# Optimization experiments

Measured on AMD Instinct MI355X. Metric: run time of the kernel, lower is better.

The kernel has to match this reference:

```python
import jax, jax.numpy as jnp
import numpy as np
from jax import lax

B, T, C, H, N = 4, 1024, 2048, 32, 64
KVH = 8            # kv heads -> kv_dim = 512, n_rep = 4
GN_EPS = 0.00064   # group_norm eps from Step3


def _l2norm(x):
    # torch F.normalize(p=2, dim=-1) with eps=1e-12
    n = jnp.linalg.norm(x, axis=-1, keepdims=True)
    return x / jnp.maximum(n, 1e-12)


def _rwkv7_scan(r, decay, k, v, aa, bb, state):
    # all inputs (B,T,H,N); state (B,H,N,N) with layout [value, key]
    def step(S, inp):
        r_t, d_t, k_t, v_t, a_t, b_t = inp  # each (B,H,N)
        sa = jnp.einsum('bhik,bhk->bhi', S, a_t)
        S = (S * d_t[:, :, None, :]
             + sa[..., None] * b_t[:, :, None, :]
             + v_t[..., None] * k_t[:, :, None, :])
        y = jnp.einsum('bhik,bhk->bhi', S, r_t)
        return S, y
    xs = tuple(jnp.moveaxis(t, 1, 0) for t in (r, decay, k, v, aa, bb))  # (T,B,H,N)
    state, ys = lax.scan(step, state, xs)
    return jnp.moveaxis(ys, 0, 1), state  # (B,T,H,N), (B,H,N,N)


def _forward(x, v_first, state, R, R_bias, K, K_bias, V, V_bias, O, O_bias,
             w0, w1, w2, a0, a1, a2, v0, v1, v2, k_k, k_a, r_k, ln_w, ln_b):
    # ---- Step1: projections + gates (hybrid_matmul -> plain matmul in fp32 ref) ----
    r = x @ R.T + R_bias                                   # (B,T,C)
    w_raw = -jax.nn.softplus(-(w0 + jnp.tanh(x @ w1) @ w2)) - 0.6
    k = x @ K.T + K_bias                                   # (B,T,512)
    v = x @ V.T + V_bias
    n_rep = C // K.shape[0]
    k = jnp.repeat(k.reshape(B, T, KVH, N), n_rep, axis=2).reshape(B, T, C)
    v = jnp.repeat(v.reshape(B, T, KVH, N), n_rep, axis=2).reshape(B, T, C)
    a = jax.nn.sigmoid(a0 + (x @ a1) @ a2)
    kk = _l2norm((k * k_k).reshape(B, T, H, N)).reshape(B, T, C)
    k = k * (1.0 + (a - 1.0) * k_a)
    # layer_id != 0: cross-layer value blending
    v = v + (v_first - v) * jax.nn.sigmoid(v0 + (x @ v1) @ v2)
    aa = -kk
    bb = kk * a
    # ---- Step2: fused recurrent rwkv7 (fp32 state) ----
    decay = jnp.exp(-jnp.exp(w_raw.astype(jnp.float32)))
    rs = lambda t: t.astype(jnp.float32).reshape(B, T, H, N)
    y, state_out = _rwkv7_scan(rs(r), decay.reshape(B, T, H, N), rs(k), rs(v), rs(aa), rs(bb), state)
    # ---- Step3: group norm over (T, N) per (batch, head) as in the (B,C,T) permute ----
    mean = y.mean(axis=(1, 3), keepdims=True)
    var = ((y - mean) ** 2).mean(axis=(1, 3), keepdims=True)
    yn = (y - mean) * lax.rsqrt(var + GN_EPS)
    xx = (yn * ln_w.reshape(H, N) + ln_b.reshape(H, N)).reshape(B, T, C)
    bonus = ((r.reshape(B, T, H, N) * k.reshape(B, T, H, N) * r_k.reshape(H, N))
             .sum(-1, keepdims=True) * v.reshape(B, T, H, N)).reshape(B, T, C)
    xx = xx + bonus
    out = xx @ O.T + O_bias
    return out


def setup_inputs() -> dict:
    key = jax.random.key(0)
    ks = jax.random.split(key, 25)
    g = lambda i, shape, s: jax.random.normal(ks[i], shape, dtype=jnp.float32) * s
    return {
        'x': g(0, (B, T, C), 1.0),
        'v_first': g(1, (B, T, C), 1.0),
        'state': jnp.zeros((B, H, N, N), dtype=jnp.float32),
        'R': g(2, (C, C), 0.02), 'R_bias': jnp.zeros((C,), jnp.float32),
        'K': g(3, (KVH * N, C), 0.02), 'K_bias': jnp.zeros((KVH * N,), jnp.float32),
        'V': g(4, (KVH * N, C), 0.02), 'V_bias': jnp.zeros((KVH * N,), jnp.float32),
        'O': g(5, (C, C), 0.02), 'O_bias': jnp.zeros((C,), jnp.float32),
        'w0': g(6, (C,), 0.1), 'w1': g(7, (C, 64), 0.05), 'w2': g(8, (64, C), 0.05),
        'a0': g(9, (C,), 0.1), 'a1': g(10, (C, 64), 0.05), 'a2': g(11, (64, C), 0.05),
        'v0': g(12, (C,), 0.1), 'v1': g(13, (C, 32), 0.05), 'v2': g(14, (32, C), 0.05),
        'k_k': 1.0 + g(15, (C,), 0.05),
        'k_a': 1.0 + g(16, (C,), 0.05),
        'r_k': g(17, (C,), 0.1),
        'ln_w': jnp.ones((C,), jnp.float32),
        'ln_b': jnp.zeros((C,), jnp.float32),
    }


def reference(x, v_first, state, R, R_bias, K, K_bias, V, V_bias, O, O_bias,
              w0, w1, w2, a0, a1, a2, v0, v1, v2, k_k, k_a, r_k, ln_w, ln_b):
    return _forward(x, v_first, state, R, R_bias, K, K_bias, V, V_bias, O, O_bias,
                    w0, w1, w2, a0, a1, a2, v0, v1, v2, k_k, k_a, r_k, ln_w, ln_b)
```

## Files before the change

### kernel.cpp

```cpp
#include <hip/hip_runtime.h>
#include <hip/hip_bf16.h>
#include <math.h>

typedef __attribute__((ext_vector_type(8))) short bf16x8;
typedef __attribute__((ext_vector_type(4))) float f32x4;

__device__ __forceinline__ unsigned short f2b(float f) {
  unsigned u = __float_as_uint(f);
  unsigned r = (u + 0x7FFF + ((u >> 16) & 1)) >> 16;
  return (unsigned short)r;
}

__device__ __forceinline__ void async16(const void* g, void* l) {
  __builtin_amdgcn_global_load_lds(
      (const __attribute__((address_space(1))) unsigned int*)(g),
      (__attribute__((address_space(3))) unsigned int*)(l), 16, 0, 0);
}

__device__ __forceinline__ float rowsum16(float x) {
  x += __int_as_float(__builtin_amdgcn_update_dpp(0, __float_as_int(x), 0x121, 0xF, 0xF, false));
  x += __int_as_float(__builtin_amdgcn_update_dpp(0, __float_as_int(x), 0x122, 0xF, 0xF, false));
  x += __int_as_float(__builtin_amdgcn_update_dpp(0, __float_as_int(x), 0x124, 0xF, 0xF, false));
  x += __int_as_float(__builtin_amdgcn_update_dpp(0, __float_as_int(x), 0x128, 0xF, 0xF, false));
  return x;
}

__global__ __launch_bounds__(256) void cvt4_kernel(
    const float* __restrict__ x, const float* __restrict__ R,
    const float* __restrict__ K, const float* __restrict__ V,
    unsigned short* __restrict__ xb, unsigned short* __restrict__ RKVb)
{
  const int bid = blockIdx.x;
  const float* s; unsigned short* d; int i;
  if (bid < 8192)       { s = x; d = xb; i = bid * 256 + threadIdx.x; }
  else if (bid < 12288) { s = R; d = RKVb; i = (bid - 8192) * 256 + threadIdx.x; }
  else if (bid < 13312) { s = K; d = RKVb + 2048 * 2048; i = (bid - 12288) * 256 + threadIdx.x; }
  else                  { s = V; d = RKVb + 2560 * 2048; i = (bid - 13312) * 256 + threadIdx.x; }
  float4 v = ((const float4*)s)[i];
  ushort4 o;
  o.x = f2b(v.x); o.y = f2b(v.y); o.z = f2b(v.z); o.w = f2b(v.w);
  ((ushort4*)d)[i] = o;
}

__global__ __launch_bounds__(256) void cvt_bf16(
    const float* __restrict__ s, unsigned short* __restrict__ d, int n4)
{
  int i = blockIdx.x * 256 + threadIdx.x;
  if (i < n4) {
    float4 v = ((const float4*)s)[i];
    ushort4 o;
    o.x = f2b(v.x); o.y = f2b(v.y); o.z = f2b(v.z); o.w = f2b(v.w);
    ((ushort4*)d)[i] = o;
  }
}

__global__ __launch_bounds__(256) void tcvt_all(
    const float* __restrict__ w1, const float* __restrict__ a1,
    const float* __restrict__ v1, const float* __restrict__ w2,
    const float* __restrict__ a2, const float* __restrict__ v2,
    unsigned short* __restrict__ Bcat, unsigned short* __restrict__ w2t,
    unsigned short* __restrict__ a2t, unsigned short* __restrict__ v2t)
{
  const int r = blockIdx.x >> 5, i = blockIdx.x & 31;
  const float* in; unsigned short* out; int Kd, Nd, ors, bx, by;
  switch (r) {
    case 0:  in = w1; out = Bcat;             Kd = 2048; Nd = 64;   ors = 2048; bx = 0; by = i; break;
    case 1:  in = a1; out = Bcat + 64 * 2048; Kd = 2048; Nd = 64;   ors = 2048; bx = 0; by = i; break;
    case 2:  in = v1; out = Bcat + 128 * 2048; Kd = 2048; Nd = 32;  ors = 2048; bx = 0; by = i; break;
    case 3:  in = w2; out = w2t;              Kd = 64;   Nd = 2048; ors = 64;   bx = i; by = 0; break;
    case 4:  in = a2; out = a2t;              Kd = 64;   Nd = 2048; ors = 64;   bx = i; by = 0; break;
    default: in = v2; out = v2t;              Kd = 32;   Nd = 2048; ors = 32;   bx = i; by = 0; break;
  }
  __shared__ unsigned short tile[64][65];
  const int tx = threadIdx.x & 63, ty = threadIdx.x >> 6;
  const int n0 = bx * 64, k0 = by * 64;
  #pragma unroll
  for (int j = 0; j < 16; ++j) {
    const int k = k0 + j * 4 + ty;
    const int n = n0 + tx;
    unsigned short v = 0;
    if (k < Kd && n < Nd) v = f2b(in[(size_t)k * Nd + n]);
    tile[j * 4 + ty][tx] = v;
  }
  __syncthreads();
  #pragma unroll
  for (int j = 0; j < 16; ++j) {
    const int n = n0 + j * 4 + ty;
    const int k = k0 + tx;
    if (n < Nd && k < Kd) out[(size_t)n * ors + k] = tile[tx][j * 4 + ty];
  }
}

template<int OUTBF16, int ACT>
__global__ __launch_bounds__(256) void gemm_mfma(
    const unsigned short* __restrict__ A, int lda,
    const unsigned short* __restrict__ B, int ldb,
    const float* __restrict__ bias, void* __restrict__ Cv, int ldc,
    int M, int N, int K)
{
  __shared__ __align__(16) unsigned short As[128 * 32];
  __shared__ __align__(16) unsigned short Bs[128 * 32];
  const int tid = threadIdx.x;
  const int w = tid >> 6, lane = tid & 63;
  const int wr = (w >> 1) * 64, wc = (w & 1) * 64;
  const int row0 = blockIdx.y * 128, col0 = blockIdx.x * 128;

  f32x4 acc[4][4];
  #pragma unroll
  for (int i = 0; i < 4; ++i)
    #pragma unroll
    for (int j = 0; j < 4; ++j)
      acc[i][j] = (f32x4){0.f, 0.f, 0.f, 0.f};

  const int srow = w * 32 + (lane >> 2);
  const int scol = (lane & 3) * 8;
  const int brow0 = (col0 + srow < N) ? (col0 + srow) : 0;
  const int brow1 = (col0 + srow + 16 < N) ? (col0 + srow + 16) : 0;
  const unsigned short* gA0 = A + (size_t)(row0 + srow) * lda + scol;
  const unsigned short* gA1 = gA0 + (size_t)16 * lda;
  const unsigned short* gB0 = B + (size_t)brow0 * ldb + scol;
  const unsigned short* gB1 = B + (size_t)brow1 * ldb + scol;
  unsigned short* lA0 = As + w * 1024;
  unsigned short* lA1 = As + w * 1024 + 512;
  unsigned short* lB0 = Bs + w * 1024;
  unsigned short* lB1 = Bs + w * 1024 + 512;

  const int m16 = lane & 15;
  const int q8  = (lane >> 4) * 8;

  for (int k0 = 0; k0 < K; k0 += 32) {
    async16(gA0, lA0);
    async16(gA1, lA1);
    async16(gB0, lB0);
    async16(gB1, lB1);
    gA0 += 32; gA1 += 32; gB0 += 32; gB1 += 32;
    __syncthreads();
    bf16x8 af[4], bfr[4];
    #pragma unroll
    for (int i = 0; i < 4; ++i) {
      af[i]  = *(const bf16x8*)(As + (wr + i * 16 + m16) * 32 + q8);
      bfr[i] = *(const bf16x8*)(Bs + (wc + i * 16 + m16) * 32 + q8);
    }
    #pragma unroll
    for (int i = 0; i < 4; ++i)
      #pragma unroll
      for (int j = 0; j < 4; ++j)
        acc[i][j] = __builtin_amdgcn_mfma_f32_16x16x32_bf16(af[i], bfr[j], acc[i][j], 0, 0, 0);
    __syncthreads();
  }

  #pragma unroll
  for (int j = 0; j < 4; ++j) {
    const int c_ = col0 + wc + j * 16 + (lane & 15);
    if (c_ < N) {
      const float bv = bias ? bias[c_] : 0.f;
      #pragma unroll
      for (int i = 0; i < 4; ++i) {
        const int r_ = row0 + wr + i * 16 + (lane >> 4) * 4;
        #pragma unroll
        for (int t4 = 0; t4 < 4; ++t4) {
          float v = acc[i][j][t4] + bv;
          if (ACT == 2 && c_ < 64) v = tanhf(v);
          if (OUTBF16)
            ((unsigned short*)Cv)[(size_t)(r_ + t4) * ldc + c_] = f2b(v);
          else
            ((float*)Cv)[(size_t)(r_ + t4) * ldc + c_] = v;
        }
      }
    }
  }
}

__global__ __launch_bounds__(256) void gemm_rkv(
    const unsigned short* __restrict__ A, const unsigned short* __restrict__ B,
    const float* __restrict__ Rb_, const float* __restrict__ Kb_,
    const float* __restrict__ Vb_,
    float* __restrict__ Cr, float* __restrict__ Ck, float* __restrict__ Cvv)
{
  __shared__ __align__(16) unsigned short As[128 * 32];
  __shared__ __align__(16) unsigned short Bs[128 * 32];
  const int tid = threadIdx.x;
  const int w = tid >> 6, lane = tid & 63;
  const int wr = (w >> 1) * 64, wc = (w & 1) * 64;
  const int row0 = blockIdx.y * 128, col0 = blockIdx.x * 128;

  float* Cd; int ldc, cbase; const float* bias;
  if (col0 < 2048)      { Cd = Cr;  ldc = 2048; cbase = col0;        bias = Rb_; }
  else if (col0 < 2560) { Cd = Ck;  ldc = 512;  cbase = col0 - 2048; bias = Kb_; }
  else                  { Cd = Cvv; ldc = 512;  cbase = col0 - 2560; bias = Vb_; }

  f32x4 acc[4][4];
  #pragma unroll
  for (int i = 0; i < 4; ++i)
    #pragma unroll
    for (int j = 0; j < 4; ++j)
      acc[i][j] = (f32x4){0.f, 0.f, 0.f, 0.f};

  const int srow = w * 32 + (lane >> 2);
  const int scol = (lane & 3) * 8;
  const unsigned short* gA0 = A + (size_t)(row0 + srow) * 2048 + scol;
  const unsigned short* gA1 = gA0 + (size_t)16 * 2048;
  const unsigned short* gB0 = B + (size_t)(col0 + srow) * 2048 + scol;
  const unsigned short* gB1 = gB0 + (size_t)16 * 2048;
  unsigned short* lA0 = As + w * 1024;
  unsigned short* lA1 = As + w * 1024 + 512;
  unsigned short* lB0 = Bs + w * 1024;
  unsigned short* lB1 = Bs + w * 1024 + 512;

  const int m16 = lane & 15;
  const int q8  = (lane >> 4) * 8;

  for (int k0 = 0; k0 < 2048; k0 += 32) {
    async16(gA0, lA0);
    async16(gA1, lA1);
    async16(gB0, lB0);
    async16(gB1, lB1);
    gA0 += 32; gA1 += 32; gB0 += 32; gB1 += 32;
    __syncthreads();
    bf16x8 af[4], bfr[4];
    #pragma unroll
    for (int i = 0; i < 4; ++i) {
      af[i]  = *(const bf16x8*)(As + (wr + i * 16 + m16) * 32 + q8);
      bfr[i] = *(const bf16x8*)(Bs + (wc + i * 16 + m16) * 32 + q8);
    }
    #pragma unroll
    for (int i = 0; i < 4; ++i)
      #pragma unroll
      for (int j = 0; j < 4; ++j)
        acc[i][j] = __builtin_amdgcn_mfma_f32_16x16x32_bf16(af[i], bfr[j], acc[i][j], 0, 0, 0);
    __syncthreads();
  }

  #pragma unroll
  for (int j = 0; j < 4; ++j) {
    const int c_ = cbase + wc + j * 16 + (lane & 15);
    const float bv = bias[c_];
    #pragma unroll
    for (int i = 0; i < 4; ++i) {
      const int r_ = row0 + wr + i * 16 + (lane >> 4) * 4;
      #pragma unroll
      for (int t4 = 0; t4 < 4; ++t4)
        Cd[(size_t)(r_ + t4) * ldc + c_] = acc[i][j][t4] + bv;
    }
  }
}

__global__ __launch_bounds__(256) void prep_kernel(
    const float* __restrict__ k_buf, const float* __restrict__ v_buf,
    const float* __restrict__ r_buf,
    float* wt_decay, const float* __restrict__ at, float* vt_vf,
    const float* __restrict__ v_first,
    const float* __restrict__ w0, const float* __restrict__ a0,
    const float* __restrict__ v0, const float* __restrict__ k_k,
    const float* __restrict__ k_a,
    unsigned* __restrict__ rk_pk, unsigned* __restrict__ ab_pk)
{
  const int row = blockIdx.x;
  const int tid = threadIdx.x;
  const int c0 = tid << 3;
  const int h = tid >> 3;
  const int kvoff = (h >> 2) << 6;
  const size_t base = (size_t)row * 2048;
  const size_t kvrow = (size_t)row * 512;
  float kr[8], kkr[8];
  float ss = 0.f;
  #pragma unroll
  for (int e = 0; e < 8; ++e) {
    const int c = c0 + e;
    const float kv = k_buf[kvrow + kvoff + (c & 63)];
    kr[e] = kv;
    const float t = kv * k_k[c];
    kkr[e] = t;
    ss = fmaf(t, t, ss);
  }
  ss += __shfl_xor(ss, 1);
  ss += __shfl_xor(ss, 2);
  ss += __shfl_xor(ss, 4);
  const float inv = 1.f / fmaxf(sqrtf(ss), 1e-12f);
  #pragma unroll
  for (int e = 0; e < 8; ++e) {
    const int c = c0 + e;
    const size_t idx = base + c;
    const float kk = kkr[e] * inv;
    const float a = 1.f / (1.f + expf(-(a0[c] + at[idx])));
    const float u = w0[c] + wt_decay[idx];
    const float sig_u = 1.f / (1.f + expf(-u));
    wt_decay[idx] = expf(-0.5488116360940264f * sig_u);
    const float kfin = kr[e] * fmaf(a - 1.f, k_a[c], 1.f);
    const float vr = v_buf[kvrow + kvoff + (c & 63)];
    const float sv = 1.f / (1.f + expf(-(v0[c] + vt_vf[idx])));
    vt_vf[idx] = vr + (v_first[idx] - vr) * sv;
    rk_pk[idx] = ((unsigned)f2b(kfin) << 16) | (unsigned)f2b(r_buf[idx]);
    ab_pk[idx] = ((unsigned)f2b(-kk) << 16) | (unsigned)f2b(kk * a);
  }
}

#define WB(n) asm volatile("s_waitcnt vmcnt(" #n ") lgkmcnt(0)\n\ts_barrier" ::: "memory")
#define BAR2() asm volatile("s_waitcnt lgkmcnt(0)\n\ts_barrier" ::: "memory")

__global__ __launch_bounds__(256) void scan_kernel(
    const unsigned* __restrict__ rkB, const unsigned* __restrict__ abB,
    const float* __restrict__ dB, const float* __restrict__ vB,
    const float* __restrict__ state, float* __restrict__ y,
    float* __restrict__ part)
{
  __shared__ float lds[6912];
  unsigned* ldsU = (unsigned*)lds;
  const int tid = threadIdx.x;
  const int bid = blockIdx.x;
  const int xcd = bid & 7, bj = bid >> 3;
  const int m = bj & 3, gq = bj >> 2;
  const int bh = (gq << 3) | xcd;
  const int widx = tid >> 6;
  const int lane = tid & 63;
  const int rg = lane >> 4;
  const int colg = lane & 15;
  const int rowb = (widx << 2) + rg;
  const int row = (m << 4) + rowb;
  const int b = bh >> 5, h = bh & 31;

  float4 S = *(const float4*)(state + (size_t)bh * 4096 + row * 64 + (colg << 2));

  const unsigned cb = (unsigned)((b * 1024) * 2048 + h * 64);
  const unsigned sstep = (unsigned)(tid >> 4);
  const unsigned scol = (unsigned)((tid & 15) << 2);
  const unsigned lseg = (unsigned)(widx << 8);

  float sacc = 0.f, ssacc = 0.f;

  #define STAGE(step0, bofs) do {                                            \
    const unsigned go_ = cb + ((step0) + sstep) * 2048u + scol;              \
    async16(rkB + go_, ldsU + (bofs) + lseg);                                \
    async16(abB + go_, ldsU + (bofs) + 1024 + lseg);                         \
    async16(dB + go_,  lds + (bofs) + 2048 + lseg);                          \
    if (lane < 16) {                                                         \
      const unsigned gv_ = cb + ((step0) + (unsigned)(widx << 2)             \
                                 + (unsigned)(lane >> 2)) * 2048u            \
                           + (unsigned)(m << 4) + (unsigned)((lane & 3) << 2); \
      async16(vB + gv_, lds + (bofs) + 3072 + (widx << 6));                  \
    }                                                                        \
  } while (0)

  #define PROCESS(bofs) do {                                                 \
    _Pragma("unroll")                                                        \
    for (int s = 0; s < 16; ++s) {                                           \
      const uint4 rkw = *(const uint4*)(ldsU + (bofs) + s * 64 + (colg << 2)); \
      const uint4 abw = *(const uint4*)(ldsU + (bofs) + 1024 + s * 64 + (colg << 2)); \
      const float4 dv = *(const float4*)(lds + (bofs) + 2048 + s * 64 + (colg << 2)); \
      const float vv = lds[(bofs) + 3072 + (s << 4) + rowb];                 \
      const float aa0 = __uint_as_float(abw.x & 0xffff0000u);                \
      const float aa1 = __uint_as_float(abw.y & 0xffff0000u);                \
      const float aa2 = __uint_as_float(abw.z & 0xffff0000u);                \
      const float aa3 = __uint_as_float(abw.w & 0xffff0000u);                \
      const float bb0 = __uint_as_float(abw.x << 16);                        \
      const float bb1 = __uint_as_float(abw.y << 16);                        \
      const float bb2 = __uint_as_float(abw.z << 16);                        \
      const float bb3 = __uint_as_float(abw.w << 16);                        \
      const float k0 = __uint_as_float(rkw.x & 0xffff0000u);                 \
      const float k1 = __uint_as_float(rkw.y & 0xffff0000u);                 \
      const float k2 = __uint_as_float(rkw.z & 0xffff0000u);                 \
      const float k3 = __uint_as_float(rkw.w & 0xffff0000u);                 \
      const float r0 = __uint_as_float(rkw.x << 16);                         \
      const float r1 = __uint_as_float(rkw.y << 16);                         \
      const float r2 = __uint_as_float(rkw.z << 16);                         \
      const float r3 = __uint_as_float(rkw.w << 16);                         \
      float t0 = fmaf(S.y, aa1, S.x * aa0);                                  \
      t0 = fmaf(S.z, aa2, t0);                                               \
      t0 = fmaf(S.w, aa3, t0);                                               \
      const float sa = rowsum16(t0);                                         \
      S.x = fmaf(S.x, dv.x, fmaf(sa, bb0, vv * k0));                         \
      S.y = fmaf(S.y, dv.y, fmaf(sa, bb1, vv * k1));                         \
      S.z = fmaf(S.z, dv.z, fmaf(sa, bb2, vv * k2));                         \
      S.w = fmaf(S.w, dv.w, fmaf(sa, bb3, vv * k3));                         \
      float t1 = fmaf(S.y, r1, S.x * r0);                                    \
      t1 = fmaf(S.z, r2, t1);                                                \
      t1 = fmaf(S.w, r3, t1);                                                \
      const float yv = rowsum16(t1);                                         \
      if (colg == 0) {                                                       \
        lds[6656 + (s << 4) + rowb] = yv;                                    \
        sacc += yv;                                                          \
        ssacc = fmaf(yv, yv, ssacc);                                         \
      }                                                                      \
    }                                                                        \
  } while (0)

  #define YSTORE(step0) do {                                                 \
    const float val_ = lds[6656 + tid];                                      \
    y[cb + ((step0) + (unsigned)(tid >> 4)) * 2048u +                        \
      (unsigned)(m << 4) + (unsigned)(tid & 15)] = val_;                     \
  } while (0)

  STAGE(0u, 0);
  STAGE(16u, 3328);

  WB(4);
  PROCESS(0);
  BAR2();
  YSTORE(0u);
  STAGE(32u, 0);

  for (int c = 1; c <= 62; ++c) {
    const int bofs = (c & 1) ? 3328 : 0;
    WB(5);
    PROCESS(bofs);
    BAR2();
    YSTORE((unsigned)(c << 4));
    if (c < 62) STAGE((unsigned)((c + 2) << 4), bofs);
  }

  WB(1);
  PROCESS(3328);
  BAR2();
  YSTORE(1008u);

  sacc  += __shfl_xor(sacc, 16);
  sacc  += __shfl_xor(sacc, 32);
  ssacc += __shfl_xor(ssacc, 16);
  ssacc += __shfl_xor(ssacc, 32);
  __syncthreads();
  if (lane == 0) { lds[widx] = sacc; lds[4 + widx] = ssacc; }
  __syncthreads();
  if (tid == 0) {
    const float s_  = lds[0] + lds[1] + lds[2] + lds[3];
    const float ss_ = lds[4] + lds[5] + lds[6] + lds[7];
    ((float2*)part)[(bh << 2) + m] = make_float2(s_, ss_);
  }

  #undef STAGE
  #undef PROCESS
  #undef YSTORE
}

__global__ __launch_bounds__(256) void gapply_kernel(
    const float* __restrict__ y, const unsigned* __restrict__ rkB,
    const float* __restrict__ vf,
    const float* __restrict__ part, const float* __restrict__ r_k,
    const float* __restrict__ ln_w, const float* __restrict__ ln_b,
    unsigned short* __restrict__ xxb)
{
  const int row = blockIdx.x;
  const int b = row >> 10;
  const int tid = threadIdx.x;
  const int h = tid >> 3;
  const int bh = b * 32 + h;
  float s = 0.f, ss = 0.f;
  #pragma unroll
  for (int j = 0; j < 4; ++j) {
    const float2 pr = ((const float2*)part)[(bh << 2) + j];
    s += pr.x; ss += pr.y;
  }
  const float mean = s * (1.f / 65536.f);
  const float rstd = rsqrtf(ss * (1.f / 65536.f) - mean * mean + 0.00064f);
  const int c0 = tid << 3;
  const size_t base = (size_t)row * 2048 + c0;
  float yv[8], vv[8];
  float p = 0.f;
  #pragma unroll
  for (int e = 0; e < 8; ++e) {
    yv[e] = y[base + e];
    vv[e] = vf[base + e];
    const unsigned w_ = rkB[base + e];
    const float rr = __uint_as_float(w_ << 16);
    const float kk_ = __uint_as_float(w_ & 0xffff0000u);
    p = fmaf(rr * kk_, r_k[c0 + e], p);
  }
  p += __shfl_xor(p, 1);
  p += __shfl_xor(p, 2);
  p += __shfl_xor(p, 4);
  #pragma unroll
  for (int e = 0; e < 8; ++e) {
    const float yn = (yv[e] - mean) * rstd;
    xxb[base + e] = f2b(fmaf(yn, ln_w[c0 + e], ln_b[c0 + e]) + p * vv[e]);
  }
}

extern "C" void kernel_launch(void* const* d_in, const int* in_sizes, int n_in,
                              void* d_out, int out_size, void* d_ws, size_t ws_size,
                              hipStream_t stream) {
  const float* x       = (const float*)d_in[0];
  const float* v_first = (const float*)d_in[1];
  const float* state   = (const float*)d_in[2];
  const float* Rw      = (const float*)d_in[3];
  const float* R_bias  = (const float*)d_in[4];
  const float* Kw      = (const float*)d_in[5];
  const float* K_bias  = (const float*)d_in[6];
  const float* Vw      = (const float*)d_in[7];
  const float* V_bias  = (const float*)d_in[8];
  const float* Ow      = (const float*)d_in[9];
  const float* O_bias  = (const float*)d_in[10];
  const float* w0      = (const float*)d_in[11];
  const float* w1      = (const float*)d_in[12];
  const float* w2      = (const float*)d_in[13];
  const float* a0      = (const float*)d_in[14];
  const float* a1      = (const float*)d_in[15];
  const float* a2      = (const float*)d_in[16];
  const float* v0      = (const float*)d_in[17];
  const float* v1      = (const float*)d_in[18];
  const float* v2      = (const float*)d_in[19];
  const float* k_k     = (const float*)d_in[20];
  const float* k_a     = (const float*)d_in[21];
  const float* r_k     = (const float*)d_in[22];
  const float* ln_w    = (const float*)d_in[23];
  const float* ln_b    = (const float*)d_in[24];

  float* ws = (float*)d_ws;
  float* r_buf = ws;
  float* k_buf = r_buf + 8388608;
  float* v_buf = k_buf + 2097152;
  float* wt    = v_buf + 2097152;
  float* at    = wt    + 8388608;
  float* vt    = at    + 8388608;
  float* kf    = vt    + 8388608;
  float* aaq   = kf    + 8388608;
  float* bbq   = aaq   + 8388608;
  float* part  = bbq   + 8388608;
  unsigned short* xb   = (unsigned short*)bbq;
  unsigned short* RKVb = (unsigned short*)kf;
  unsigned short* hcat = (unsigned short*)(kf + 3200000);
  unsigned short* Bcat = (unsigned short*)(kf + 3600000);
  unsigned short* w2t  = (unsigned short*)(kf + 3800000);
  unsigned short* a2t  = (unsigned short*)(kf + 3900000);
  unsigned short* v2t  = (unsigned short*)(kf + 4000000);
  unsigned* rk_pk      = (unsigned*)aaq;
  unsigned* ab_pk      = (unsigned*)bbq;
  unsigned short* Ob   = (unsigned short*)wt;
  unsigned short* xxb  = (unsigned short*)bbq;

  dim3 blk(256);
  cvt4_kernel<<<14336, blk, 0, stream>>>(x, Rw, Kw, Vw, xb, RKVb);
  tcvt_all<<<192, blk, 0, stream>>>(w1, a1, v1, w2, a2, v2, Bcat, w2t, a2t, v2t);
  gemm_mfma<1,2><<<dim3(2, 32), blk, 0, stream>>>(xb, 2048, Bcat, 2048, nullptr,
                                                  hcat, 160, 4096, 160, 2048);
  gemm_rkv<<<dim3(24, 32), blk, 0, stream>>>(xb, RKVb, R_bias, K_bias, V_bias,
                                             r_buf, k_buf, v_buf);
  gemm_mfma<0,0><<<dim3(16, 32), blk, 0, stream>>>(hcat, 160, w2t, 64, nullptr,
                                                   wt, 2048, 4096, 2048, 64);
  gemm_mfma<0,0><<<dim3(16, 32), blk, 0, stream>>>(hcat + 64, 160, a2t, 64, nullptr,
                                                   at, 2048, 4096, 2048, 64);
  gemm_mfma<0,0><<<dim3(16, 32), blk, 0, stream>>>(hcat + 128, 160, v2t, 32, nullptr,
                                                   vt, 2048, 4096, 2048, 32);
  prep_kernel<<<4096, blk, 0, stream>>>(k_buf, v_buf, r_buf, wt, at, vt, v_first,
                                        w0, a0, v0, k_k, k_a, rk_pk, ab_pk);
  float* ybuf = at;
  scan_kernel<<<512, blk, 0, stream>>>(rk_pk, ab_pk, wt, vt, state, ybuf, part);
  cvt_bf16<<<4096, blk, 0, stream>>>(Ow, Ob, 1048576);
  gapply_kernel<<<4096, blk, 0, stream>>>(ybuf, rk_pk, vt, part, r_k,
                                          ln_w, ln_b, xxb);
  gemm_mfma<0,0><<<dim3(16, 32), blk, 0, stream>>>(xxb, 2048, Ob, 2048, O_bias,
                                                   (float*)d_out, 2048, 4096, 2048, 2048);
}
```

Before: 765.6 us.

## Pack scan operands as fp16 and use v_fma_mix; merge three low-rank GEMM launches

The packed r/k and a/b operands change from bf16 to fp16 via v_cvt_pkrtz, and the scan inner loop now uses v_fma_mix_f32 to consume the packed halves directly. This removes the shift/mask unpacking instructions on the serial recurrence path. The three small low-rank second-stage GEMMs are merged into one launch using a z grid dimension, cutting launch overhead. fp16 has less range than bf16 and pkrtz rounds toward zero, which could change accuracy.

```diff
diff --git a/kernel.cpp b/kernel.cpp
--- a/kernel.cpp
+++ b/kernel.cpp
@@ -23,6 +23,22 @@
   x += __int_as_float(__builtin_amdgcn_update_dpp(0, __float_as_int(x), 0x124, 0xF, 0xF, false));
   x += __int_as_float(__builtin_amdgcn_update_dpp(0, __float_as_int(x), 0x128, 0xF, 0xF, false));
   return x;
+}
+
+__device__ __forceinline__ float mixhi(float a, unsigned pk, float c) {
+  float d;
+  asm("v_fma_mix_f32 %0, %1, %2, %3 op_sel:[0,1,0] op_sel_hi:[0,1,0]"
+      : "=v"(d) : "v"(a), "v"(pk), "v"(c));
+  return d;
+}
+__device__ __forceinline__ float mixlo(float a, unsigned pk, float c) {
+  float d;
+  asm("v_fma_mix_f32 %0, %1, %2, %3 op_sel:[0,0,0] op_sel_hi:[0,1,0]"
+      : "=v"(d) : "v"(a), "v"(pk), "v"(c));
+  return d;
+}
+__device__ __forceinline__ float h2f(unsigned h) {
+  float f; asm("v_cvt_f32_f16 %0, %1" : "=v"(f) : "v"(h)); return f;
 }
 
 __global__ __launch_bounds__(256) void cvt4_kernel(
@@ -92,18 +108,17 @@
 }
 
 template<int OUTBF16, int ACT>
-__global__ __launch_bounds__(256) void gemm_mfma(
+__device__ __forceinline__ void gemm_body(
     const unsigned short* __restrict__ A, int lda,
     const unsigned short* __restrict__ B, int ldb,
     const float* __restrict__ bias, void* __restrict__ Cv, int ldc,
-    int M, int N, int K)
+    int M, int N, int K, int row0, int col0)
 {
   __shared__ __align__(16) unsigned short As[128 * 32];
   __shared__ __align__(16) unsigned short Bs[128 * 32];
   const int tid = threadIdx.x;
   const int w = tid >> 6, lane = tid & 63;
   const int wr = (w >> 1) * 64, wc = (w & 1) * 64;
-  const int row0 = blockIdx.y * 128, col0 = blockIdx.x * 128;
 
   f32x4 acc[4][4];
   #pragma unroll
@@ -171,23 +186,50 @@
   }
 }
 
+template<int OUTBF16, int ACT>
+__global__ __launch_bounds__(256) void gemm_mfma(
+    const unsigned short* __restrict__ A, int lda,
+    const unsigned short* __restrict__ B, int ldb,
+    const float* __restrict__ bias, void* __restrict__ Cv, int ldc,
+    int M, int N, int K)
+{
+  gemm_body<OUTBF16, ACT>(A, lda, B, ldb, bias, Cv, ldc, M, N, K,
+                          blockIdx.y * 128, blockIdx.x * 128);
+}
+
+__global__ __launch_bounds__(256) void gemm_lr2(
+    const unsigned short* __restrict__ hcat,
+    const unsigned short* __restrict__ w2t,
+    const unsigned short* __restrict__ a2t,
+    const unsigned short* __restrict__ v2t,
+    float* __restrict__ wt, float* __restrict__ at, float* __restrict__ vt)
+{
+  const int z = blockIdx.z;
+  const unsigned short* A; const unsigned short* Bm; float* C; int K;
+  if (z == 0)      { A = hcat;       Bm = w2t; C = wt; K = 64; }
+  else if (z == 1) { A = hcat + 64;  Bm = a2t; C = at; K = 64; }
+  else             { A = hcat + 128; Bm = v2t; C = vt; K = 32; }
+  gemm_body<0, 0>(A, 160, Bm, K, nullptr, C, 2048, 4096, 2048, K,
+                  blockIdx.y * 128, blockIdx.x * 128);
+}
+
 __global__ __launch_bounds__(256) void gemm_rkv(
     const unsigned short* __restrict__ A, const unsigned short* __restrict__ B,
     const float* __restrict__ Rb_, const float* __restrict__ Kb_,
     const float* __restrict__ Vb_,
     float* __restrict__ Cr, float* __restrict__ Ck, float* __restrict__ Cvv)
 {
+  const int col0 = blockIdx.x * 128;
+  float* Cd; int ldc, cbase; const float* bias;
+  if (col0 < 2048)      { Cd = Cr;  ldc = 2048; cbase = col0;        bias = Rb_; }
+  else if (col0 < 2560) { Cd = Ck;  ldc = 512;  cbase = col0 - 2048; bias = Kb_; }
+  else                  { Cd = Cvv; ldc = 512;  cbase = col0 - 2560; bias = Vb_; }
   __shared__ __align__(16) unsigned short As[128 * 32];
   __shared__ __align__(16) unsigned short Bs[128 * 32];
   const int tid = threadIdx.x;
   const int w = tid >> 6, lane = tid & 63;
   const int wr = (w >> 1) * 64, wc = (w & 1) * 64;
-  const int row0 = blockIdx.y * 128, col0 = blockIdx.x * 128;
-
-  float* Cd; int ldc, cbase; const float* bias;
-  if (col0 < 2048)      { Cd = Cr;  ldc = 2048; cbase = col0;        bias = Rb_; }
-  else if (col0 < 2560) { Cd = Ck;  ldc = 512;  cbase = col0 - 2048; bias = Kb_; }
-  else                  { Cd = Cvv; ldc = 512;  cbase = col0 - 2560; bias = Vb_; }
+  const int row0 = blockIdx.y * 128;
 
   f32x4 acc[4][4];
   #pragma unroll
@@ -290,8 +332,13 @@
     const float vr = v_buf[kvrow + kvoff + (c & 63)];
     const float sv = 1.f / (1.f + expf(-(v0[c] + vt_vf[idx])));
     vt_vf[idx] = vr + (v_first[idx] - vr) * sv;
-    rk_pk[idx] = ((unsigned)f2b(kfin) << 16) | (unsigned)f2b(r_buf[idx]);
-    ab_pk[idx] = ((unsigned)f2b(-kk) << 16) | (unsigned)f2b(kk * a);
+    const float bbv = kk * a;
+    const float aav = -kk;
+    unsigned rk_u, ab_u;
+    asm("v_cvt_pkrtz_f16_f32 %0, %1, %2" : "=v"(rk_u) : "v"(r_buf[idx]), "v"(kfin));
+    asm("v_cvt_pkrtz_f16_f32 %0, %1, %2" : "=v"(ab_u) : "v"(bbv), "v"(aav));
+    rk_pk[idx] = rk_u;
+    ab_pk[idx] = ab_u;
   }
 }
 
@@ -327,6 +374,7 @@
   const unsigned lseg = (unsigned)(widx << 8);
 
   float sacc = 0.f, ssacc = 0.f;
+  const float fzero = 0.0f;
 
   #define STAGE(step0, bofs) do {                                            \
     const unsigned go_ = cb + ((step0) + sstep) * 2048u + scol;              \
@@ -348,33 +396,27 @@
       const uint4 abw = *(const uint4*)(ldsU + (bofs) + 1024 + s * 64 + (colg << 2)); \
       const float4 dv = *(const float4*)(lds + (bofs) + 2048 + s * 64 + (colg << 2)); \
       const float vv = lds[(bofs) + 3072 + (s << 4) + rowb];                 \
-      const float aa0 = __uint_as_float(abw.x & 0xffff0000u);                \
-      const float aa1 = __uint_as_float(abw.y & 0xffff0000u);                \
-      const float aa2 = __uint_as_float(abw.z & 0xffff0000u);                \
-      const float aa3 = __uint_as_float(abw.w & 0xffff0000u);                \
-      const float bb0 = __uint_as_float(abw.x << 16);                        \
-      const float bb1 = __uint_as_float(abw.y << 16);                        \
-      const float bb2 = __uint_as_float(abw.z << 16);                        \
-      const float bb3 = __uint_as_float(abw.w << 16);                        \
-      const float k0 = __uint_as_float(rkw.x & 0xffff0000u);                 \
-      const float k1 = __uint_as_float(rkw.y & 0xffff0000u);                 \
-      const float k2 = __uint_as_float(rkw.z & 0xffff0000u);                 \
-      const float k3 = __uint_as_float(rkw.w & 0xffff0000u);                 \
-      const float r0 = __uint_as_float(rkw.x << 16);                         \
-      const float r1 = __uint_as_float(rkw.y << 16);                         \
-      const float r2 = __uint_as_float(rkw.z << 16);                         \
-      const float r3 = __uint_as_float(rkw.w << 16);                         \
-      float t0 = fmaf(S.y, aa1, S.x * aa0);                                  \
-      t0 = fmaf(S.z, aa2, t0);                                               \
-      t0 = fmaf(S.w, aa3, t0);                                               \
+      float t0 = mixhi(S.x, abw.x, fzero);                                   \
+      t0 = mixhi(S.y, abw.y, t0);                                            \
+      t0 = mixhi(S.z, abw.z, t0);                                            \
+      t0 = mixhi(S.w, abw.w, t0);                                            \
       const float sa = rowsum16(t0);                                         \
-      S.x = fmaf(S.x, dv.x, fmaf(sa, bb0, vv * k0));                         \
-      S.y = fmaf(S.y, dv.y, fmaf(sa, bb1, vv * k1));                         \
-      S.z = fmaf(S.z, dv.z, fmaf(sa, bb2, vv * k2));                         \
-      S.w = fmaf(S.w, dv.w, fmaf(sa, bb3, vv * k3));                         \
-      float t1 = fmaf(S.y, r1, S.x * r0);                                    \
-      t1 = fmaf(S.z, r2, t1);                                                \
-      t1 = fmaf(S.w, r3, t1);                                                \
+      float p0 = mixhi(vv, rkw.x, fzero);                                    \
+      float p1 = mixhi(vv, rkw.y, fzero);                                    \
+      float p2 = mixhi(vv, rkw.z, fzero);                                    \
+      float p3 = mixhi(vv, rkw.w, fzero);                                    \
+      p0 = mixlo(sa, abw.x, p0);                                             \
+      p1 = mixlo(sa, abw.y, p1);                                             \
+      p2 = mixlo(sa, abw.z, p2);                                             \
+      p3 = mixlo(sa, abw.w, p3);                                             \
+      S.x = fmaf(S.x, dv.x, p0);                                             \
+      S.y = fmaf(S.y, dv.y, p1);                                             \
+      S.z = fmaf(S.z, dv.z, p2);                                             \
+      S.w = fmaf(S.w, dv.w, p3);                                             \
+      float t1 = mixlo(S.x, rkw.x, fzero);                                   \
+      t1 = mixlo(S.y, rkw.y, t1);                                            \
+      t1 = mixlo(S.z, rkw.z, t1);                                            \
+      t1 = mixlo(S.w, rkw.w, t1);                                            \
       const float yv = rowsum16(t1);                                         \
       if (colg == 0) {                                                       \
         lds[6656 + (s << 4) + rowb] = yv;                                    \
@@ -460,9 +502,7 @@
     yv[e] = y[base + e];
     vv[e] = vf[base + e];
     const unsigned w_ = rkB[base + e];
-    const float rr = __uint_as_float(w_ << 16);
-    const float kk_ = __uint_as_float(w_ & 0xffff0000u);
-    p = fmaf(rr * kk_, r_k[c0 + e], p);
+    p = fmaf(h2f(w_ & 0xffffu) * h2f(w_ >> 16), r_k[c0 + e], p);
   }
   p += __shfl_xor(p, 1);
   p += __shfl_xor(p, 2);
@@ -533,12 +573,7 @@
                                                   hcat, 160, 4096, 160, 2048);
   gemm_rkv<<<dim3(24, 32), blk, 0, stream>>>(xb, RKVb, R_bias, K_bias, V_bias,
                                              r_buf, k_buf, v_buf);
-  gemm_mfma<0,0><<<dim3(16, 32), blk, 0, stream>>>(hcat, 160, w2t, 64, nullptr,
-                                                   wt, 2048, 4096, 2048, 64);
-  gemm_mfma<0,0><<<dim3(16, 32), blk, 0, stream>>>(hcat + 64, 160, a2t, 64, nullptr,
-                                                   at, 2048, 4096, 2048, 64);
-  gemm_mfma<0,0><<<dim3(16, 32), blk, 0, stream>>>(hcat + 128, 160, v2t, 32, nullptr,
-                                                   vt, 2048, 4096, 2048, 32);
+  gemm_lr2<<<dim3(16, 32, 3), blk, 0, stream>>>(hcat, w2t, a2t, v2t, wt, at, vt);
   prep_kernel<<<4096, blk, 0, stream>>>(k_buf, v_buf, r_buf, wt, at, vt, v_first,
                                         w0, a0, v0, k_k, k_a, rk_pk, ab_pk);
   float* ybuf = at;
```

Result: faster. 748.4 us (-2.2%).
